# Performance work log

Hardware: AMD Instinct MI355X
Metric: run time of the kernel (lower is better)

Reference implementation:

```python
import jax, jax.numpy as jnp
import numpy as np

B, N, D, T = 32768, 20, 172, 100
E = D + T          # MHA embed dim = 272
H = 2              # num heads
HD = E // H        # head dim = 136
MEM = 172


def setup_inputs() -> dict:
    key = jax.random.key(0)
    ks = jax.random.split(key, 16)
    s = 0.02
    return {
        "message_batch": jax.random.normal(ks[0], (B, N, D), jnp.float32),
        "time_batch": jax.random.normal(ks[1], (B, N), jnp.float32),
        "memory": jax.random.normal(ks[2], (B, MEM), jnp.float32),
        # TimeEncode: Linear(1, T) -> weight [T], bias [T], output cos(w*t+b)
        "time_w": jax.random.normal(ks[3], (T,), jnp.float32),
        "time_b": jax.random.normal(ks[4], (T,), jnp.float32),
        # nn.MultiheadAttention(embed_dim=E, num_heads=2)
        "in_proj_w": jax.random.normal(ks[5], (3 * E, E), jnp.float32) * s,
        "in_proj_b": jnp.zeros((3 * E,), jnp.float32),
        "out_proj_w": jax.random.normal(ks[6], (E, E), jnp.float32) * s,
        "out_proj_b": jnp.zeros((E,), jnp.float32),
        # MergeLayer(E, D, D, D): fc1 Linear(E+D, D), fc2 Linear(D, D)
        "fc1_w": jax.random.normal(ks[7], (D, E + D), jnp.float32) * s,
        "fc1_b": jnp.zeros((D,), jnp.float32),
        "fc2_w": jax.random.normal(ks[8], (D, D), jnp.float32) * s,
        "fc2_b": jnp.zeros((D,), jnp.float32),
    }


def reference(message_batch, time_batch, memory, time_w, time_b,
              in_proj_w, in_proj_b, out_proj_w, out_proj_b,
              fc1_w, fc1_b, fc2_w, fc2_b):
    # --- aggregate() batched core (use_age=False) ---
    mask = time_batch < 0                              # [B,N] key_padding_mask (True = pad)
    source_time = time_batch[:, -1:]                   # [B,1]
    delta = time_batch - source_time                   # [B,N]
    # TimeEncode: cos(Linear(1->T))
    time_feat = jnp.cos(delta[..., None] * time_w + time_b)   # [B,N,T]

    # --- attention_node.forward ---
    msgs_un = jnp.concatenate([message_batch, time_feat], axis=-1)  # [B,N,E]
    source = message_batch[:, -1, :]                   # [B,D] (reassigned; memory unused for output)
    Q = jnp.concatenate([source, time_feat[:, -1, :]], axis=-1)    # [B,E]

    invalid = mask.all(axis=1)                         # [B] all-padded rows
    mask = mask.at[:, 0].set(jnp.where(invalid, False, mask[:, 0]))

    # nn.MultiheadAttention (self K=V)
    wq, wk, wv = in_proj_w[:E], in_proj_w[E:2 * E], in_proj_w[2 * E:]
    bq, bk, bv = in_proj_b[:E], in_proj_b[E:2 * E], in_proj_b[2 * E:]
    q = (Q @ wq.T + bq).reshape(B, H, HD)              # [B,H,hd]
    k = (msgs_un @ wk.T + bk).reshape(B, N, H, HD)     # [B,N,H,hd]
    v = (msgs_un @ wv.T + bv).reshape(B, N, H, HD)

    scale = 1.0 / jnp.sqrt(jnp.asarray(HD, q.dtype))
    scores = jnp.einsum("bhd,bnhd->bhn", q, k) * scale  # [B,H,N]
    neg = jnp.asarray(-1e9, scores.dtype)
    scores = jnp.where(mask[:, None, :], neg, scores)
    attn = jax.nn.softmax(scores, axis=-1)
    ctx = jnp.einsum("bhn,bnhd->bhd", attn, v).reshape(B, E)
    attn_out = ctx @ out_proj_w.T + out_proj_b          # [B,E]
    attn_out = jnp.where(invalid[:, None], 0.0, attn_out)

    # MergeLayer: fc2(relu(fc1(cat(attn_out, source))))
    h = jax.nn.relu(jnp.concatenate([attn_out, source], axis=-1) @ fc1_w.T + fc1_b)
    out = h @ fc2_w.T + fc2_b                           # [B,D] aggregated messages
    return out
```

## Files before the change

### kernel.cpp

```cpp
#include <hip/hip_runtime.h>
#include <math.h>

#define BB 32768
#define BN 20
#define DD 172
#define TT 100
#define EE 272
#define HD2 136
#define BT 16

#define XLD 448
#define QLD 548
#define NQK 546
#define GBM 128
#define GBN 128
#define GBK 64

#define GSWZ(k) ((((k) >> 3) & 7) << 2)

__global__ __launch_bounds__(256, 2)
void gemm_f32(const float* __restrict__ A, int lda,
              const float* __restrict__ W, int ldw,
              const float* __restrict__ bias,
              float* __restrict__ C, int ldc,
              int N, int K, int act, const int* __restrict__ inval)
{
  __shared__ float As[GBK][GBM + 4];
  __shared__ float Ws[GBK][GBN + 4];
  const int t  = threadIdx.x;
  const int bm = blockIdx.x * GBM;
  const int bn = blockIdx.y * GBN;
  const int tx = t & 15, ty = t >> 4;
  const int c4 = (t & 15) * 4;
  const int g4 = (t >> 4) * 4;

  float acc[8][8];
#pragma unroll
  for (int i = 0; i < 8; i++)
#pragma unroll
    for (int j = 0; j < 8; j++) acc[i][j] = 0.f;

  for (int kt = 0; kt < K; kt += GBK) {
    const int kg = kt + c4;
    const bool kv = (kg < K);
    const int sw = GSWZ(c4);

#pragma unroll
    for (int p = 0; p < 2; p++) {
      const int m0 = g4 + p * 64;
      float4 v0 = make_float4(0.f,0.f,0.f,0.f), v1 = v0, v2 = v0, v3 = v0;
      if (kv) {
        const float* ap = A + (size_t)(bm + m0) * lda + kg;
        v0 = *(const float4*)(ap);
        v1 = *(const float4*)(ap + lda);
        v2 = *(const float4*)(ap + 2 * (size_t)lda);
        v3 = *(const float4*)(ap + 3 * (size_t)lda);
      }
      const int ms = m0 ^ sw;
      *(float4*)&As[c4 + 0][ms] = make_float4(v0.x, v1.x, v2.x, v3.x);
      *(float4*)&As[c4 + 1][ms] = make_float4(v0.y, v1.y, v2.y, v3.y);
      *(float4*)&As[c4 + 2][ms] = make_float4(v0.z, v1.z, v2.z, v3.z);
      *(float4*)&As[c4 + 3][ms] = make_float4(v0.w, v1.w, v2.w, v3.w);
    }
#pragma unroll
    for (int p = 0; p < 2; p++) {
      const int n0 = g4 + p * 64;
      float4 v0 = make_float4(0.f,0.f,0.f,0.f), v1 = v0, v2 = v0, v3 = v0;
      if (kv) {
        const float* wp = W + (size_t)(bn + n0) * ldw + kg;
        if (bn + n0 + 0 < N) v0 = *(const float4*)(wp);
        if (bn + n0 + 1 < N) v1 = *(const float4*)(wp + ldw);
        if (bn + n0 + 2 < N) v2 = *(const float4*)(wp + 2 * (size_t)ldw);
        if (bn + n0 + 3 < N) v3 = *(const float4*)(wp + 3 * (size_t)ldw);
      }
      const int ns = n0 ^ sw;
      *(float4*)&Ws[c4 + 0][ns] = make_float4(v0.x, v1.x, v2.x, v3.x);
      *(float4*)&Ws[c4 + 1][ns] = make_float4(v0.y, v1.y, v2.y, v3.y);
      *(float4*)&Ws[c4 + 2][ns] = make_float4(v0.z, v1.z, v2.z, v3.z);
      *(float4*)&Ws[c4 + 3][ns] = make_float4(v0.w, v1.w, v2.w, v3.w);
    }
    __syncthreads();

#pragma unroll 4
    for (int k = 0; k < GBK; k++) {
      const int s = GSWZ(k);
      const float4 a0 = *(const float4*)&As[k][(ty * 4) ^ s];
      const float4 a1 = *(const float4*)&As[k][(64 + ty * 4) ^ s];
      const float4 b0 = *(const float4*)&Ws[k][(tx * 4) ^ s];
      const float4 b1 = *(const float4*)&Ws[k][(64 + tx * 4) ^ s];
      const float av[8] = {a0.x, a0.y, a0.z, a0.w, a1.x, a1.y, a1.z, a1.w};
      const float bv[8] = {b0.x, b0.y, b0.z, b0.w, b1.x, b1.y, b1.z, b1.w};
#pragma unroll
      for (int i = 0; i < 8; i++)
#pragma unroll
        for (int j = 0; j < 8; j++)
          acc[i][j] = fmaf(av[i], bv[j], acc[i][j]);
    }
    __syncthreads();
  }

#pragma unroll
  for (int i = 0; i < 8; i++) {
    const int row = bm + ((i < 4) ? (ty * 4 + i) : (64 + ty * 4 + i - 4));
    const int zr = (act == 2) ? inval[row] : 0;
#pragma unroll
    for (int jh = 0; jh < 2; jh++) {
      const int n0 = bn + jh * 64 + tx * 4;
      if (n0 < N) {
        const float4 bs = *(const float4*)(bias + n0);
        float4 v = make_float4(acc[i][jh * 4 + 0] + bs.x,
                               acc[i][jh * 4 + 1] + bs.y,
                               acc[i][jh * 4 + 2] + bs.z,
                               acc[i][jh * 4 + 3] + bs.w);
        if (act == 1) {
          v.x = fmaxf(v.x, 0.f); v.y = fmaxf(v.y, 0.f);
          v.z = fmaxf(v.z, 0.f); v.w = fmaxf(v.w, 0.f);
        }
        if (zr) { v.x = 0.f; v.y = 0.f; v.z = 0.f; v.w = 0.f; }
        *(float4*)(C + (size_t)row * ldc + n0) = v;
      }
    }
  }
}

__global__ __launch_bounds__(256)
void kprep0(const float* __restrict__ ipw, const float* __restrict__ ipb,
            const float* __restrict__ opw, const float* __restrict__ opb,
            const float* __restrict__ tbg,
            float* __restrict__ qconst, float* __restrict__ cvo)
{
  for (int e = threadIdx.x; e < EE; e += 256) {
    float s = ipb[e];
    for (int u = 0; u < TT; u++)
      s += cosf(tbg[u]) * ipw[(size_t)e * EE + DD + u];
    qconst[e] = s;
    float s2 = opb[e];
    for (int c = 0; c < EE; c++)
      s2 += ipb[2 * EE + c] * opw[(size_t)e * EE + c];
    cvo[e] = s2;
  }
}

#define NT1 (NQK * DD)
#define NT2 (NT1 + NQK)
#define NT3 (NT2 + EE * 2 * EE)

__global__ __launch_bounds__(256)
void kprep1(const float* __restrict__ ipw, const float* __restrict__ ipb,
            const float* __restrict__ opw, const float* __restrict__ qconst,
            float* __restrict__ wqk, float* __restrict__ cqk,
            float* __restrict__ wvo)
{
  for (int idx = blockIdx.x * 256 + threadIdx.x; idx < NT3;
       idx += gridDim.x * 256) {
    if (idx < NT1) {
      const int n = idx / DD, k = idx % DD;
      const int h = n / 273, j = n % 273;
      const float* wa = ipw + (size_t)(h * HD2) * EE + k;
      float s = 0.f;
      if (j < EE) {
        const float* wb = ipw + (size_t)(EE + h * HD2) * EE + j;
        for (int d = 0; d < HD2; d++) s += wa[(size_t)d * EE] * wb[(size_t)d * EE];
      } else {
        const float* bb = ipb + EE + h * HD2;
        for (int d = 0; d < HD2; d++) s += wa[(size_t)d * EE] * bb[d];
      }
      wqk[idx] = s;
    } else if (idx < NT2) {
      const int n = idx - NT1;
      const int h = n / 273, j = n % 273;
      const float* qc = qconst + h * HD2;
      float s = 0.f;
      if (j < EE) {
        const float* wb = ipw + (size_t)(EE + h * HD2) * EE + j;
        for (int d = 0; d < HD2; d++) s += qc[d] * wb[(size_t)d * EE];
      } else {
        const float* bb = ipb + EE + h * HD2;
        for (int d = 0; d < HD2; d++) s += qc[d] * bb[d];
      }
      cqk[n] = s;
    } else {
      const int r = idx - NT2;
      const int e = r / (2 * EE), kk = r % (2 * EE);
      const int h = kk / EE, j = kk % EE;
      const float* wv = ipw + (size_t)(2 * EE + h * HD2) * EE + j;
      const float* wo = opw + (size_t)e * EE + h * HD2;
      float s = 0.f;
      for (int d = 0; d < HD2; d++) s += wv[(size_t)d * EE] * wo[d];
      wvo[r] = s;
    }
  }
}

__global__ __launch_bounds__(256)
void ksrc(const float* __restrict__ msg, float* __restrict__ xbuf)
{
  const int total = BB * DD;
  for (int idx = blockIdx.x * 256 + threadIdx.x; idx < total;
       idx += gridDim.x * 256) {
    const int i = idx / DD, d = idx % DD;
    xbuf[(size_t)i * XLD + EE + d] =
        msg[((size_t)i * BN + (BN - 1)) * DD + d];
  }
}

__global__ __launch_bounds__(256, 2)
void attn_mid(const float* __restrict__ msg,
              const float* __restrict__ timeb,
              const float* __restrict__ twg,
              const float* __restrict__ tbg,
              float* __restrict__ qkbuf,
              int* __restrict__ inval)
{
  __shared__ float s_red[4][16][41];
  __shared__ float s_sc[4][40];
  const int t = threadIdx.x;
  const int w = t >> 6, l = t & 63;
  const size_t i = (size_t)blockIdx.x * 4 + w;

  const float* tbr = timeb + i * BN;
  float d[BN];
  unsigned msk = 0;
  const float st = tbr[BN - 1];
#pragma unroll
  for (int n = 0; n < BN; n++) {
    const float v = tbr[n];
    if (v < 0.f) msk |= (1u << n);
    d[n] = v - st;
  }
  const int inv = (msk == ((1u << BN) - 1u)) ? 1 : 0;
  if (inv) msk &= ~1u;

  const float w0 = twg[l], b0 = tbg[l];
  float w1 = 0.f, b1 = 0.f;
  if (l < TT - 64) { w1 = twg[64 + l]; b1 = tbg[64 + l]; }

  float* qkr = qkbuf + i * QLD;
  float qm0[2], qm1[2], qm2[2], qt0[2], qt1[2], sct[2];
#pragma unroll
  for (int h = 0; h < 2; h++) {
    const float* q = qkr + h * 273;
    qm0[h] = q[l];
    qm1[h] = q[64 + l];
    qm2[h] = (l < DD - 128) ? q[128 + l] : 0.f;
    qt0[h] = q[DD + l];
    qt1[h] = (l < TT - 64) ? q[DD + 64 + l] : 0.f;
    sct[h] = q[272];
  }

  const float* mrow = msg + i * (size_t)(BN * DD);
  float acc[2][BN];
#pragma unroll
  for (int n = 0; n < BN; n++) { acc[0][n] = 0.f; acc[1][n] = 0.f; }
#pragma unroll
  for (int n = 0; n < BN; n++) {
    const float m0 = mrow[n * DD + l];
    const float m1 = mrow[n * DD + 64 + l];
    const float m2 = (l < DD - 128) ? mrow[n * DD + 128 + l] : 0.f;
    const float c0 = __cosf(d[n] * w0 + b0);
    const float c1 = __cosf(d[n] * w1 + b1);
    acc[0][n] += m0 * qm0[0] + m1 * qm1[0] + m2 * qm2[0] + c0 * qt0[0] + c1 * qt1[0];
    acc[1][n] += m0 * qm0[1] + m1 * qm1[1] + m2 * qm2[1] + c0 * qt0[1] + c1 * qt1[1];
  }

  float* af = &acc[0][0];
#pragma unroll
  for (int x = 0; x < 40; x++) {
    float v = af[x];
    v += __shfl_xor(v, 32);
    v += __shfl_xor(v, 16);
    af[x] = v;
  }
  if (l < 16) {
#pragma unroll
    for (int x = 0; x < 40; x++) s_red[w][l][x] = af[x];
  }
  __syncthreads();
  if (l < 40) {
    float s = 0.f;
#pragma unroll
    for (int q = 0; q < 16; q++) s += s_red[w][q][l];
    const int h = (l >= BN) ? 1 : 0;
    const int n = l - h * BN;
    s += sct[h];
    s *= 0.08574929257125442f;
    if ((msk >> n) & 1u) s = -1e9f;
    s_sc[w][l] = s;
  }
  __syncthreads();

  float p[40];
#pragma unroll
  for (int x = 0; x < 40; x += 4) {
    const float4 v4 = *(const float4*)&s_sc[w][x];
    p[x] = v4.x; p[x + 1] = v4.y; p[x + 2] = v4.z; p[x + 3] = v4.w;
  }
#pragma unroll
  for (int h = 0; h < 2; h++) {
    float mx = p[h * BN];
#pragma unroll
    for (int n = 1; n < BN; n++) mx = fmaxf(mx, p[h * BN + n]);
    float sm = 0.f;
#pragma unroll
    for (int n = 0; n < BN; n++) {
      const float e = __expf(p[h * BN + n] - mx);
      p[h * BN + n] = e; sm += e;
    }
    const float is = 1.f / sm;
#pragma unroll
    for (int n = 0; n < BN; n++) p[h * BN + n] *= is;
  }

  float a0[2] = {0.f, 0.f}, a1[2] = {0.f, 0.f}, a2[2] = {0.f, 0.f};
  float t0[2] = {0.f, 0.f}, t1[2] = {0.f, 0.f};
#pragma unroll
  for (int n = 0; n < BN; n++) {
    const float m0 = mrow[n * DD + l];
    const float m1 = mrow[n * DD + 64 + l];
    const float m2 = (l < DD - 128) ? mrow[n * DD + 128 + l] : 0.f;
    const float c0 = __cosf(d[n] * w0 + b0);
    const float c1 = __cosf(d[n] * w1 + b1);
#pragma unroll
    for (int h = 0; h < 2; h++) {
      const float at = p[h * BN + n];
      a0[h] = fmaf(at, m0, a0[h]);
      a1[h] = fmaf(at, m1, a1[h]);
      a2[h] = fmaf(at, m2, a2[h]);
      t0[h] = fmaf(at, c0, t0[h]);
      t1[h] = fmaf(at, c1, t1[h]);
    }
  }
#pragma unroll
  for (int h = 0; h < 2; h++) {
    float* o = qkr + h * EE;
    o[l] = a0[h];
    o[64 + l] = a1[h];
    if (l < DD - 128) o[128 + l] = a2[h];
    o[DD + l] = t0[h];
    if (l < TT - 64) o[DD + 64 + l] = t1[h];
  }
  if (l == 0) inval[i] = inv;
}

__device__ __forceinline__ void gemm_rowW(
    const float* __restrict__ W, int ldw, int kcol0,
    const float* __restrict__ bias,
    const float* __restrict__ A, int lda,
    int K,
    float* OUT, int ldo, int NO,
    bool accum, int act,
    const int* __restrict__ inval,
    float* __restrict__ gout, int gld,
    int t)
{
  const int eo = t & 63;
  const int i0 = (t >> 6) * 4;
  for (int e = eo; e < NO; e += 128) {
    const int e2 = e + 64;
    const bool has2 = (e2 < NO);
    float acc[4][2];
    const float b1 = (!accum && bias) ? bias[e] : 0.f;
    const float b2 = (!accum && bias && has2) ? bias[e2] : 0.f;
#pragma unroll
    for (int ii = 0; ii < 4; ii++) {
      acc[ii][0] = accum ? OUT[(i0 + ii) * ldo + e] : b1;
      acc[ii][1] = has2 ? (accum ? OUT[(i0 + ii) * ldo + e2] : b2) : 0.f;
    }
    const float* w1 = W + (size_t)e * ldw + kcol0;
    const float* w2 = W + (size_t)e2 * ldw + kcol0;
    for (int k = 0; k < K; k += 4) {
      const float4 wq1 = *(const float4*)(w1 + k);
      float4 wq2 = make_float4(0.f, 0.f, 0.f, 0.f);
      if (has2) wq2 = *(const float4*)(w2 + k);
#pragma unroll
      for (int ii = 0; ii < 4; ii++) {
        const float4 a = *(const float4*)(A + (size_t)(i0 + ii) * lda + k);
        acc[ii][0] += a.x * wq1.x + a.y * wq1.y + a.z * wq1.z + a.w * wq1.w;
        acc[ii][1] += a.x * wq2.x + a.y * wq2.y + a.z * wq2.z + a.w * wq2.w;
      }
    }
#pragma unroll
    for (int ii = 0; ii < 4; ii++) {
      float v1 = acc[ii][0], v2 = acc[ii][1];
      if (act == 1) { v1 = fmaxf(v1, 0.f); v2 = fmaxf(v2, 0.f); }
      else if (act == 2) { if (inval[i0 + ii]) { v1 = 0.f; v2 = 0.f; } }
      if (gout) {
        gout[(i0 + ii) * gld + e] = v1;
        if (has2) gout[(i0 + ii) * gld + e2] = v2;
      } else {
        OUT[(i0 + ii) * ldo + e] = v1;
        if (has2) OUT[(i0 + ii) * ldo + e2] = v2;
      }
    }
  }
}

__device__ __forceinline__ void gemm_colW(
    const float* __restrict__ W, int ldw,
    const float* __restrict__ A, int lda,
    int K,
    float* OUT, int ldo, int NO,
    int t)
{
  const int eo = t & 63;
  const int i0 = (t >> 6) * 4;
  for (int j = eo; j < NO; j += 128) {
    const int j2 = j + 64;
    const bool has2 = (j2 < NO);
    float acc[4][2];
#pragma unroll
    for (int ii = 0; ii < 4; ii++) { acc[ii][0] = 0.f; acc[ii][1] = 0.f; }
    for (int dd = 0; dd < K; dd += 4) {
      const float* wr = W + (size_t)dd * ldw;
      const float w10 = wr[j];
      const float w11 = wr[ldw + j];
      const float w12 = wr[2 * ldw + j];
      const float w13 = wr[3 * ldw + j];
      float w20 = 0.f, w21 = 0.f, w22 = 0.f, w23 = 0.f;
      if (has2) { w20 = wr[j2]; w21 = wr[ldw + j2]; w22 = wr[2 * ldw + j2]; w23 = wr[3 * ldw + j2]; }
#pragma unroll
      for (int ii = 0; ii < 4; ii++) {
        const float4 a = *(const float4*)(A + (size_t)(i0 + ii) * lda + dd);
        acc[ii][0] += a.x * w10 + a.y * w11 + a.z * w12 + a.w * w13;
        acc[ii][1] += a.x * w20 + a.y * w21 + a.z * w22 + a.w * w23;
      }
    }
#pragma unroll
    for (int ii = 0; ii < 4; ii++) {
      OUT[(i0 + ii) * ldo + j] = acc[ii][0];
      if (has2) OUT[(i0 + ii) * ldo + j2] = acc[ii][1];
    }
  }
}

__global__ __launch_bounds__(256, 2)
void attn_msg_agg_fused(const float* __restrict__ msg,
                        const float* __restrict__ timeb,
                        const float* __restrict__ tw_g,
                        const float* __restrict__ tb_g,
                        const float* __restrict__ ipw,
                        const float* __restrict__ ipb,
                        const float* __restrict__ opw,
                        const float* __restrict__ opb,
                        const float* __restrict__ f1w,
                        const float* __restrict__ f1b,
                        const float* __restrict__ f2w,
                        const float* __restrict__ f2b,
                        float* __restrict__ outg)
{
  __shared__ __align__(16) float s_q[BT * EE];
  __shared__ __align__(16) float s_qk[BT * 2 * EE];
  __shared__ __align__(16) float s_attn[BT * 2 * BN];
  __shared__ __align__(16) float s_delta[BT * BN];
  __shared__ __align__(16) float s_tw[TT];
  __shared__ __align__(16) float s_tb[TT];
  __shared__ __align__(16) float s_tfl[TT];
  __shared__ float s_sconst[BT * 2];
  __shared__ unsigned s_mask[BT];
  __shared__ int s_inval[BT];

  const int t = threadIdx.x;
  const int base = blockIdx.x * BT;

  if (t < TT) {
    const float b = tb_g[t];
    s_tw[t] = tw_g[t];
    s_tb[t] = b;
    s_tfl[t] = __cosf(b);
  }
  for (int idx = t; idx < BT * BN; idx += 256)
    s_delta[idx] = timeb[(size_t)base * BN + idx];
  __syncthreads();
  if (t < BT) {
    const float st = s_delta[t * BN + BN - 1];
    unsigned m = 0;
#pragma unroll
    for (int n = 0; n < BN; n++) {
      const float v = s_delta[t * BN + n];
      if (v < 0.f) m |= (1u << n);
      s_delta[t * BN + n] = v - st;
    }
    const int inv = (m == ((1u << BN) - 1u)) ? 1 : 0;
    if (inv) m &= ~1u;
    s_mask[t] = m;
    s_inval[t] = inv;
  }
  __syncthreads();

  const float* srcA = msg + (size_t)base * BN * DD + (size_t)(BN - 1) * DD;
  gemm_rowW(ipw, EE, 0, ipb, srcA, BN * DD, DD, s_q, EE, EE, false, 0, nullptr, nullptr, 0, t);
  gemm_rowW(ipw, EE, DD, nullptr, s_tfl, 0, TT, s_q, EE, EE, true, 0, nullptr, nullptr, 0, t);
  __syncthreads();

  if (t < BT * 2) {
    const int i = t >> 1, h = t & 1;
    const float* qv = s_q + i * EE + h * HD2;
    const float* bk = ipb + EE + h * HD2;
    float s = 0.f;
    for (int dd = 0; dd < HD2; dd++) s += qv[dd] * bk[dd];
    s_sconst[t] = s;
  }
  gemm_colW(ipw + (size_t)EE * EE, EE, s_q, EE, HD2, s_qk, 2 * EE, EE, t);
  gemm_colW(ipw + (size_t)(EE + HD2) * EE, EE, s_q + HD2, EE, HD2, s_qk + EE, 2 * EE, EE, t);
  __syncthreads();

  const float scale = 0.08574929257125442f;
  for (int o = t; o < BT * 2 * BN; o += 256) {
    const int i = o / (2 * BN);
    const int r = o % (2 * BN);
    const int h = r / BN;
    const int n = r % BN;
    const float* mrow = msg + ((size_t)(base + i) * BN + n) * DD;
    const float* qkv = s_qk + i * 2 * EE + h * EE;
    float s = s_sconst[i * 2 + h];
    for (int dd = 0; dd < DD; dd += 4) {
      const float4 m4 = *(const float4*)(mrow + dd);
      const float4 q4 = *(const float4*)(qkv + dd);
      s += m4.x * q4.x + m4.y * q4.y + m4.z * q4.z + m4.w * q4.w;
    }
    const float del = s_delta[i * BN + n];
    const float* qkt = qkv + DD;
    for (int u = 0; u < TT; u++)
      s += __cosf(del * s_tw[u] + s_tb[u]) * qkt[u];
    const bool masked = (s_mask[i] >> n) & 1u;
    s_attn[o] = masked ? -1e9f : s * scale;
  }
  __syncthreads();

  if (t < BT * 2) {
    float* sc = s_attn + t * BN;
    float m = -3.4e38f;
#pragma unroll
    for (int n = 0; n < BN; n++) m = fmaxf(m, sc[n]);
    float sum = 0.f;
#pragma unroll
    for (int n = 0; n < BN; n++) { const float e = __expf(sc[n] - m); sc[n] = e; sum += e; }
    const float inv = 1.f / sum;
#pragma unroll
    for (int n = 0; n < BN; n++) sc[n] *= inv;
  }
  __syncthreads();

  for (int o = t; o < BT * 2 * EE; o += 256) {
    const int i = o / (2 * EE);
    const int r = o % (2 * EE);
    const int h = r / EE;
    const int j = r % EE;
    const float* at = s_attn + (i * 2 + h) * BN;
    float acc = 0.f;
    if (j < DD) {
      const float* mp = msg + (size_t)(base + i) * BN * DD + j;
#pragma unroll
      for (int n = 0; n < BN; n++) acc += at[n] * mp[n * DD];
    } else {
      const int u = j - DD;
      const float ww = s_tw[u], bb = s_tb[u];
#pragma unroll
      for (int n = 0; n < BN; n++) acc += at[n] * __cosf(s_delta[i * BN + n] * ww + bb);
    }
    s_qk[o] = acc;
  }
  __syncthreads();

  gemm_rowW(ipw + (size_t)(2 * EE) * EE, EE, 0, ipb + 2 * EE,
            s_qk, 2 * EE, EE, s_q, EE, HD2, false, 0, nullptr, nullptr, 0, t);
  gemm_rowW(ipw + (size_t)(2 * EE + HD2) * EE, EE, 0, ipb + 2 * EE + HD2,
            s_qk + EE, 2 * EE, EE, s_q + HD2, EE, HD2, false, 0, nullptr, nullptr, 0, t);
  __syncthreads();

  gemm_rowW(opw, EE, 0, opb, s_q, EE, EE, s_qk, 2 * EE, EE, false, 2, s_inval, nullptr, 0, t);
  __syncthreads();

  gemm_rowW(f1w, EE + DD, 0, f1b, s_qk, 2 * EE, EE, s_q, EE, DD, false, 0, nullptr, nullptr, 0, t);
  gemm_rowW(f1w, EE + DD, EE, nullptr, srcA, BN * DD, DD, s_q, EE, DD, true, 1, nullptr, nullptr, 0, t);
  __syncthreads();

  gemm_rowW(f2w, DD, 0, f2b, s_q, EE, DD, nullptr, 0, DD, false, 0, nullptr,
            outg + (size_t)base * DD, DD, t);
}

extern "C" void kernel_launch(void* const* d_in, const int* in_sizes, int n_in,
                              void* d_out, int out_size, void* d_ws, size_t ws_size,
                              hipStream_t stream) {
  const float* msg  = (const float*)d_in[0];
  const float* tb   = (const float*)d_in[1];
  const float* tw_g = (const float*)d_in[3];
  const float* tb_g = (const float*)d_in[4];
  const float* ipw  = (const float*)d_in[5];
  const float* ipb  = (const float*)d_in[6];
  const float* opw  = (const float*)d_in[7];
  const float* opb  = (const float*)d_in[8];
  const float* f1w  = (const float*)d_in[9];
  const float* f1b  = (const float*)d_in[10];
  const float* f2w  = (const float*)d_in[11];
  const float* f2b  = (const float*)d_in[12];
  float* outg = (float*)d_out;

  const size_t F_X   = 0;
  const size_t F_QK  = F_X   + (size_t)BB * XLD;
  const size_t F_WQK = F_QK  + (size_t)BB * QLD;
  const size_t F_CQK = F_WQK + (size_t)NQK * DD;
  const size_t F_WVO = F_CQK + 548;
  const size_t F_CVO = F_WVO + (size_t)EE * 2 * EE;
  const size_t F_QC  = F_CVO + EE;
  const size_t F_INV = F_QC  + EE;
  const size_t NEEDF = F_INV + BB;

  if (ws_size >= NEEDF * sizeof(float)) {
    float* ws    = (float*)d_ws;
    float* xbuf  = ws + F_X;
    float* qkb   = ws + F_QK;
    float* wqk   = ws + F_WQK;
    float* cqk   = ws + F_CQK;
    float* wvo   = ws + F_WVO;
    float* cvo   = ws + F_CVO;
    float* qc    = ws + F_QC;
    int*   inval = (int*)(ws + F_INV);

    hipLaunchKernelGGL(kprep0, dim3(1), dim3(256), 0, stream,
                       ipw, ipb, opw, opb, tb_g, qc, cvo);
    hipLaunchKernelGGL(kprep1, dim3(512), dim3(256), 0, stream,
                       ipw, ipb, opw, qc, wqk, cqk, wvo);
    hipLaunchKernelGGL(ksrc, dim3(2048), dim3(256), 0, stream, msg, xbuf);
    hipLaunchKernelGGL(gemm_f32, dim3(BB / GBM, 5), dim3(256), 0, stream,
                       xbuf + EE, XLD, wqk, DD, cqk, qkb, QLD,
                       NQK, DD, 0, (const int*)nullptr);
    hipLaunchKernelGGL(attn_mid, dim3(BB / 4), dim3(256), 0, stream,
                       msg, tb, tw_g, tb_g, qkb, inval);
    hipLaunchKernelGGL(gemm_f32, dim3(BB / GBM, 3), dim3(256), 0, stream,
                       qkb, QLD, wvo, 2 * EE, cvo, xbuf, XLD,
                       EE, 2 * EE, 2, inval);
    hipLaunchKernelGGL(gemm_f32, dim3(BB / GBM, 2), dim3(256), 0, stream,
                       xbuf, XLD, f1w, EE + DD, f1b, qkb, DD,
                       DD, EE + DD, 1, (const int*)nullptr);
    hipLaunchKernelGGL(gemm_f32, dim3(BB / GBM, 2), dim3(256), 0, stream,
                       qkb, DD, f2w, DD, f2b, outg, DD,
                       DD, DD, 0, (const int*)nullptr);
  } else {
    dim3 grid(BB / BT), block(256);
    hipLaunchKernelGGL(attn_msg_agg_fused, grid, block, 0, stream,
                       msg, tb, tw_g, tb_g, ipw, ipb, opw, opb,
                       f1w, f1b, f2w, f2b, outg);
  }
}
```

Measured before the change: 1.178 ms.

## Fold V/out-proj into fc1 weights and add register prefetch to GEMM

Precomputes a combined weight matrix that folds the value projection, output projection and the attention half of fc1 into one [D x 720] matrix. This replaces two batch-sized GEMMs (VO then fc1) with a single one over a unified buffer holding source, a validity column and the weighted context. Invalid rows are handled by scaling the context and bias column by a validity flag instead of masking in the epilogue. The GEMM gains templated N-width and register double-buffered global loads for the next K tile, at the cost of extra prep kernels and more register pressure.

```diff
diff --git a/kernel.cpp b/kernel.cpp
--- a/kernel.cpp
+++ b/kernel.cpp
@@ -9,91 +9,117 @@
 #define HD2 136
 #define BT 16
 
-#define XLD 448
-#define QLD 548
-#define NQK 546
+#define XLD2 728
+#define KMO  720
+#define QOFF 176
+#define NQK  546
+#define HLD  176
 #define GBM 128
-#define GBN 128
 #define GBK 64
 
 #define GSWZ(k) ((((k) >> 3) & 7) << 2)
 
+template<int PW>
+__device__ __forceinline__ void g_fetch(
+    const float* __restrict__ A, int lda,
+    const float* __restrict__ W, int ldw,
+    int N, int K, int bm, int bn, int kt, int c4, int g4,
+    float4 ra[2][4], float4 rw[PW][4])
+{
+  const int kg = kt + c4;
+  const bool kv = (kg < K);
+#pragma unroll
+  for (int p = 0; p < 2; p++) {
+    if (kv) {
+      const float* ap = A + (size_t)(bm + g4 + p * 64) * lda + kg;
+      ra[p][0] = *(const float4*)(ap);
+      ra[p][1] = *(const float4*)(ap + lda);
+      ra[p][2] = *(const float4*)(ap + 2 * (size_t)lda);
+      ra[p][3] = *(const float4*)(ap + 3 * (size_t)lda);
+    } else {
+      ra[p][0] = ra[p][1] = ra[p][2] = ra[p][3] = make_float4(0.f, 0.f, 0.f, 0.f);
+    }
+  }
+#pragma unroll
+  for (int p = 0; p < PW; p++) {
+    const int n0 = g4 + p * 64;
+    rw[p][0] = rw[p][1] = rw[p][2] = rw[p][3] = make_float4(0.f, 0.f, 0.f, 0.f);
+    if (kv) {
+      const float* wp = W + (size_t)(bn + n0) * ldw + kg;
+      if (bn + n0 + 0 < N) rw[p][0] = *(const float4*)(wp);
+      if (bn + n0 + 1 < N) rw[p][1] = *(const float4*)(wp + ldw);
+      if (bn + n0 + 2 < N) rw[p][2] = *(const float4*)(wp + 2 * (size_t)ldw);
+      if (bn + n0 + 3 < N) rw[p][3] = *(const float4*)(wp + 3 * (size_t)ldw);
+    }
+  }
+}
+
+template<int PW>
 __global__ __launch_bounds__(256, 2)
 void gemm_f32(const float* __restrict__ A, int lda,
               const float* __restrict__ W, int ldw,
               const float* __restrict__ bias,
               float* __restrict__ C, int ldc,
-              int N, int K, int act, const int* __restrict__ inval)
+              int N, int K, int act)
 {
   __shared__ float As[GBK][GBM + 4];
-  __shared__ float Ws[GBK][GBN + 4];
+  __shared__ float Ws[GBK][PW * 64 + 4];
   const int t  = threadIdx.x;
   const int bm = blockIdx.x * GBM;
-  const int bn = blockIdx.y * GBN;
+  const int bn = blockIdx.y * (PW * 64);
   const int tx = t & 15, ty = t >> 4;
   const int c4 = (t & 15) * 4;
   const int g4 = (t >> 4) * 4;
-
-  float acc[8][8];
+  const int sw0 = GSWZ(c4);
+
+  float acc[8][4 * PW];
 #pragma unroll
   for (int i = 0; i < 8; i++)
 #pragma unroll
-    for (int j = 0; j < 8; j++) acc[i][j] = 0.f;
+    for (int j = 0; j < 4 * PW; j++) acc[i][j] = 0.f;
+
+  float4 ra[2][4], rw[PW][4];
+  g_fetch<PW>(A, lda, W, ldw, N, K, bm, bn, 0, c4, g4, ra, rw);
 
   for (int kt = 0; kt < K; kt += GBK) {
-    const int kg = kt + c4;
-    const bool kv = (kg < K);
-    const int sw = GSWZ(c4);
-
 #pragma unroll
     for (int p = 0; p < 2; p++) {
-      const int m0 = g4 + p * 64;
-      float4 v0 = make_float4(0.f,0.f,0.f,0.f), v1 = v0, v2 = v0, v3 = v0;
-      if (kv) {
-        const float* ap = A + (size_t)(bm + m0) * lda + kg;
-        v0 = *(const float4*)(ap);
-        v1 = *(const float4*)(ap + lda);
-        v2 = *(const float4*)(ap + 2 * (size_t)lda);
-        v3 = *(const float4*)(ap + 3 * (size_t)lda);
-      }
-      const int ms = m0 ^ sw;
-      *(float4*)&As[c4 + 0][ms] = make_float4(v0.x, v1.x, v2.x, v3.x);
-      *(float4*)&As[c4 + 1][ms] = make_float4(v0.y, v1.y, v2.y, v3.y);
-      *(float4*)&As[c4 + 2][ms] = make_float4(v0.z, v1.z, v2.z, v3.z);
-      *(float4*)&As[c4 + 3][ms] = make_float4(v0.w, v1.w, v2.w, v3.w);
-    }
-#pragma unroll
-    for (int p = 0; p < 2; p++) {
-      const int n0 = g4 + p * 64;
-      float4 v0 = make_float4(0.f,0.f,0.f,0.f), v1 = v0, v2 = v0, v3 = v0;
-      if (kv) {
-        const float* wp = W + (size_t)(bn + n0) * ldw + kg;
-        if (bn + n0 + 0 < N) v0 = *(const float4*)(wp);
-        if (bn + n0 + 1 < N) v1 = *(const float4*)(wp + ldw);
-        if (bn + n0 + 2 < N) v2 = *(const float4*)(wp + 2 * (size_t)ldw);
-        if (bn + n0 + 3 < N) v3 = *(const float4*)(wp + 3 * (size_t)ldw);
-      }
-      const int ns = n0 ^ sw;
-      *(float4*)&Ws[c4 + 0][ns] = make_float4(v0.x, v1.x, v2.x, v3.x);
-      *(float4*)&Ws[c4 + 1][ns] = make_float4(v0.y, v1.y, v2.y, v3.y);
-      *(float4*)&Ws[c4 + 2][ns] = make_float4(v0.z, v1.z, v2.z, v3.z);
-      *(float4*)&Ws[c4 + 3][ns] = make_float4(v0.w, v1.w, v2.w, v3.w);
+      const int ms = (g4 + p * 64) ^ sw0;
+      *(float4*)&As[c4 + 0][ms] = make_float4(ra[p][0].x, ra[p][1].x, ra[p][2].x, ra[p][3].x);
+      *(float4*)&As[c4 + 1][ms] = make_float4(ra[p][0].y, ra[p][1].y, ra[p][2].y, ra[p][3].y);
+      *(float4*)&As[c4 + 2][ms] = make_float4(ra[p][0].z, ra[p][1].z, ra[p][2].z, ra[p][3].z);
+      *(float4*)&As[c4 + 3][ms] = make_float4(ra[p][0].w, ra[p][1].w, ra[p][2].w, ra[p][3].w);
+    }
+#pragma unroll
+    for (int p = 0; p < PW; p++) {
+      const int ns = (g4 + p * 64) ^ sw0;
+      *(float4*)&Ws[c4 + 0][ns] = make_float4(rw[p][0].x, rw[p][1].x, rw[p][2].x, rw[p][3].x);
+      *(float4*)&Ws[c4 + 1][ns] = make_float4(rw[p][0].y, rw[p][1].y, rw[p][2].y, rw[p][3].y);
+      *(float4*)&Ws[c4 + 2][ns] = make_float4(rw[p][0].z, rw[p][1].z, rw[p][2].z, rw[p][3].z);
+      *(float4*)&Ws[c4 + 3][ns] = make_float4(rw[p][0].w, rw[p][1].w, rw[p][2].w, rw[p][3].w);
     }
     __syncthreads();
+
+    if (kt + GBK < K)
+      g_fetch<PW>(A, lda, W, ldw, N, K, bm, bn, kt + GBK, c4, g4, ra, rw);
 
 #pragma unroll 4
     for (int k = 0; k < GBK; k++) {
       const int s = GSWZ(k);
       const float4 a0 = *(const float4*)&As[k][(ty * 4) ^ s];
       const float4 a1 = *(const float4*)&As[k][(64 + ty * 4) ^ s];
+      const float av[8] = {a0.x, a0.y, a0.z, a0.w, a1.x, a1.y, a1.z, a1.w};
+      float bv[4 * PW];
       const float4 b0 = *(const float4*)&Ws[k][(tx * 4) ^ s];
-      const float4 b1 = *(const float4*)&Ws[k][(64 + tx * 4) ^ s];
-      const float av[8] = {a0.x, a0.y, a0.z, a0.w, a1.x, a1.y, a1.z, a1.w};
-      const float bv[8] = {b0.x, b0.y, b0.z, b0.w, b1.x, b1.y, b1.z, b1.w};
+      bv[0] = b0.x; bv[1] = b0.y; bv[2] = b0.z; bv[3] = b0.w;
+      if constexpr (PW == 2) {
+        const float4 b1 = *(const float4*)&Ws[k][(64 + tx * 4) ^ s];
+        bv[4] = b1.x; bv[5] = b1.y; bv[6] = b1.z; bv[7] = b1.w;
+      }
 #pragma unroll
       for (int i = 0; i < 8; i++)
 #pragma unroll
-        for (int j = 0; j < 8; j++)
+        for (int j = 0; j < 4 * PW; j++)
           acc[i][j] = fmaf(av[i], bv[j], acc[i][j]);
     }
     __syncthreads();
@@ -102,9 +128,8 @@
 #pragma unroll
   for (int i = 0; i < 8; i++) {
     const int row = bm + ((i < 4) ? (ty * 4 + i) : (64 + ty * 4 + i - 4));
-    const int zr = (act == 2) ? inval[row] : 0;
-#pragma unroll
-    for (int jh = 0; jh < 2; jh++) {
+#pragma unroll
+    for (int jh = 0; jh < PW; jh++) {
       const int n0 = bn + jh * 64 + tx * 4;
       if (n0 < N) {
         const float4 bs = *(const float4*)(bias + n0);
@@ -116,7 +141,6 @@
           v.x = fmaxf(v.x, 0.f); v.y = fmaxf(v.y, 0.f);
           v.z = fmaxf(v.z, 0.f); v.w = fmaxf(v.w, 0.f);
         }
-        if (zr) { v.x = 0.f; v.y = 0.f; v.z = 0.f; v.w = 0.f; }
         *(float4*)(C + (size_t)row * ldc + n0) = v;
       }
     }
@@ -124,36 +148,32 @@
 }
 
 __global__ __launch_bounds__(256)
-void kprep0(const float* __restrict__ ipw, const float* __restrict__ ipb,
-            const float* __restrict__ opw, const float* __restrict__ opb,
-            const float* __restrict__ tbg,
-            float* __restrict__ qconst, float* __restrict__ cvo)
+void kprepA(const float* __restrict__ ipw, const float* __restrict__ ipb,
+            const float* __restrict__ tbg, float* __restrict__ qconst)
 {
   for (int e = threadIdx.x; e < EE; e += 256) {
     float s = ipb[e];
     for (int u = 0; u < TT; u++)
       s += cosf(tbg[u]) * ipw[(size_t)e * EE + DD + u];
     qconst[e] = s;
-    float s2 = opb[e];
-    for (int c = 0; c < EE; c++)
-      s2 += ipb[2 * EE + c] * opw[(size_t)e * EE + c];
-    cvo[e] = s2;
-  }
-}
-
-#define NT1 (NQK * DD)
-#define NT2 (NT1 + NQK)
-#define NT3 (NT2 + EE * 2 * EE)
+  }
+}
+
+#define PB0 (NQK * DD)
+#define PB1 (PB0 + NQK)
+#define PB2 (PB1 + DD * EE)
 
 __global__ __launch_bounds__(256)
-void kprep1(const float* __restrict__ ipw, const float* __restrict__ ipb,
-            const float* __restrict__ opw, const float* __restrict__ qconst,
+void kprepB(const float* __restrict__ ipw, const float* __restrict__ ipb,
+            const float* __restrict__ opw, const float* __restrict__ f1w,
+            const float* __restrict__ qconst,
             float* __restrict__ wqk, float* __restrict__ cqk,
-            float* __restrict__ wvo)
-{
-  for (int idx = blockIdx.x * 256 + threadIdx.x; idx < NT3;
+            float* __restrict__ Tm)
+{
+  if (blockIdx.x == 0 && threadIdx.x < 2) cqk[NQK + threadIdx.x] = 0.f;
+  for (int idx = blockIdx.x * 256 + threadIdx.x; idx < PB2;
        idx += gridDim.x * 256) {
-    if (idx < NT1) {
+    if (idx < PB0) {
       const int n = idx / DD, k = idx % DD;
       const int h = n / 273, j = n % 273;
       const float* wa = ipw + (size_t)(h * HD2) * EE + k;
@@ -166,8 +186,8 @@
         for (int d = 0; d < HD2; d++) s += wa[(size_t)d * EE] * bb[d];
       }
       wqk[idx] = s;
-    } else if (idx < NT2) {
-      const int n = idx - NT1;
+    } else if (idx < PB1) {
+      const int n = idx - PB0;
       const int h = n / 273, j = n % 273;
       const float* qc = qconst + h * HD2;
       float s = 0.f;
@@ -180,15 +200,47 @@
       }
       cqk[n] = s;
     } else {
-      const int r = idx - NT2;
-      const int e = r / (2 * EE), kk = r % (2 * EE);
-      const int h = kk / EE, j = kk % EE;
+      const int r = idx - PB1;
+      const int o = r / EE, c = r % EE;
+      const float* fa = f1w + (size_t)o * (EE + DD);
+      const float* wb = opw + c;
+      float s = 0.f;
+      for (int e = 0; e < EE; e++) s += fa[e] * wb[(size_t)e * EE];
+      Tm[r] = s;
+    }
+  }
+}
+
+#define PCN (DD * KMO)
+
+__global__ __launch_bounds__(256)
+void kprepC(const float* __restrict__ ipw, const float* __restrict__ ipb,
+            const float* __restrict__ opb, const float* __restrict__ f1w,
+            const float* __restrict__ Tm, float* __restrict__ wmof)
+{
+  for (int idx = blockIdx.x * 256 + threadIdx.x; idx < PCN;
+       idx += gridDim.x * 256) {
+    const int o = idx / KMO, kk = idx % KMO;
+    float s;
+    if (kk < DD) {
+      s = f1w[(size_t)o * (EE + DD) + EE + kk];
+    } else if (kk == DD) {
+      const float* fa = f1w + (size_t)o * (EE + DD);
+      const float* Tr = Tm + (size_t)o * EE;
+      s = 0.f;
+      for (int e = 0; e < EE; e++) s += fa[e] * opb[e];
+      for (int c = 0; c < EE; c++) s += Tr[c] * ipb[2 * EE + c];
+    } else if (kk < QOFF) {
+      s = 0.f;
+    } else {
+      const int j2 = kk - QOFF;
+      const int h = j2 / EE, j = j2 % EE;
+      const float* Tr = Tm + (size_t)o * EE + h * HD2;
       const float* wv = ipw + (size_t)(2 * EE + h * HD2) * EE + j;
-      const float* wo = opw + (size_t)e * EE + h * HD2;
-      float s = 0.f;
-      for (int d = 0; d < HD2; d++) s += wv[(size_t)d * EE] * wo[d];
-      wvo[r] = s;
-    }
+      s = 0.f;
+      for (int d = 0; d < HD2; d++) s += Tr[d] * wv[(size_t)d * EE];
+    }
+    wmof[idx] = s;
   }
 }
 
@@ -199,8 +251,7 @@
   for (int idx = blockIdx.x * 256 + threadIdx.x; idx < total;
        idx += gridDim.x * 256) {
     const int i = idx / DD, d = idx % DD;
-    xbuf[(size_t)i * XLD + EE + d] =
-        msg[((size_t)i * BN + (BN - 1)) * DD + d];
+    xbuf[(size_t)i * XLD2 + d] = msg[((size_t)i * BN + (BN - 1)) * DD + d];
   }
 }
 
@@ -209,8 +260,7 @@
               const float* __restrict__ timeb,
               const float* __restrict__ twg,
               const float* __restrict__ tbg,
-              float* __restrict__ qkbuf,
-              int* __restrict__ inval)
+              float* __restrict__ xbuf)
 {
   __shared__ float s_red[4][16][41];
   __shared__ float s_sc[4][40];
@@ -230,12 +280,14 @@
   }
   const int inv = (msk == ((1u << BN) - 1u)) ? 1 : 0;
   if (inv) msk &= ~1u;
+  const float vf = inv ? 0.f : 1.f;
 
   const float w0 = twg[l], b0 = tbg[l];
   float w1 = 0.f, b1 = 0.f;
   if (l < TT - 64) { w1 = twg[64 + l]; b1 = tbg[64 + l]; }
 
-  float* qkr = qkbuf + i * QLD;
+  float* xrow = xbuf + i * XLD2;
+  float* qkr = xrow + QOFF;
   float qm0[2], qm1[2], qm2[2], qt0[2], qt1[2], sct[2];
 #pragma unroll
   for (int h = 0; h < 2; h++) {
@@ -333,13 +385,18 @@
 #pragma unroll
   for (int h = 0; h < 2; h++) {
     float* o = qkr + h * EE;
-    o[l] = a0[h];
-    o[64 + l] = a1[h];
-    if (l < DD - 128) o[128 + l] = a2[h];
-    o[DD + l] = t0[h];
-    if (l < TT - 64) o[DD + 64 + l] = t1[h];
-  }
-  if (l == 0) inval[i] = inv;
+    o[l] = a0[h] * vf;
+    o[64 + l] = a1[h] * vf;
+    if (l < DD - 128) o[128 + l] = a2[h] * vf;
+    o[DD + l] = t0[h] * vf;
+    if (l < TT - 64) o[DD + 64 + l] = t1[h] * vf;
+  }
+  if (l == 0) {
+    xrow[DD] = vf;
+    xrow[DD + 1] = 0.f;
+    xrow[DD + 2] = 0.f;
+    xrow[DD + 3] = 0.f;
+  }
 }
 
 __device__ __forceinline__ void gemm_rowW(
@@ -596,46 +653,43 @@
   const float* f2b  = (const float*)d_in[12];
   float* outg = (float*)d_out;
 
-  const size_t F_X   = 0;
-  const size_t F_QK  = F_X   + (size_t)BB * XLD;
-  const size_t F_WQK = F_QK  + (size_t)BB * QLD;
-  const size_t F_CQK = F_WQK + (size_t)NQK * DD;
-  const size_t F_WVO = F_CQK + 548;
-  const size_t F_CVO = F_WVO + (size_t)EE * 2 * EE;
-  const size_t F_QC  = F_CVO + EE;
-  const size_t F_INV = F_QC  + EE;
-  const size_t NEEDF = F_INV + BB;
+  const size_t F_X    = 0;
+  const size_t F_H    = F_X    + (size_t)BB * XLD2;
+  const size_t F_WQK  = F_H    + (size_t)BB * HLD;
+  const size_t F_CQK  = F_WQK  + (size_t)NQK * DD;
+  const size_t F_T    = F_CQK  + 548;
+  const size_t F_WMOF = F_T    + (size_t)DD * EE;
+  const size_t F_QC   = F_WMOF + (size_t)DD * KMO;
+  const size_t NEEDF  = F_QC   + EE;
 
   if (ws_size >= NEEDF * sizeof(float)) {
-    float* ws    = (float*)d_ws;
-    float* xbuf  = ws + F_X;
-    float* qkb   = ws + F_QK;
-    float* wqk   = ws + F_WQK;
-    float* cqk   = ws + F_CQK;
-    float* wvo   = ws + F_WVO;
-    float* cvo   = ws + F_CVO;
-    float* qc    = ws + F_QC;
-    int*   inval = (int*)(ws + F_INV);
-
-    hipLaunchKernelGGL(kprep0, dim3(1), dim3(256), 0, stream,
-                       ipw, ipb, opw, opb, tb_g, qc, cvo);
-    hipLaunchKernelGGL(kprep1, dim3(512), dim3(256), 0, stream,
-                       ipw, ipb, opw, qc, wqk, cqk, wvo);
+    float* ws   = (float*)d_ws;
+    float* xbuf = ws + F_X;
+    float* hbuf = ws + F_H;
+    float* wqk  = ws + F_WQK;
+    float* cqk  = ws + F_CQK;
+    float* Tm   = ws + F_T;
+    float* wmof = ws + F_WMOF;
+    float* qc   = ws + F_QC;
+
+    hipLaunchKernelGGL(kprepA, dim3(1), dim3(256), 0, stream,
+                       ipw, ipb, tb_g, qc);
+    hipLaunchKernelGGL(kprepB, dim3(256), dim3(256), 0, stream,
+                       ipw, ipb, opw, f1w, qc, wqk, cqk, Tm);
+    hipLaunchKernelGGL(kprepC, dim3(256), dim3(256), 0, stream,
+                       ipw, ipb, opb, f1w, Tm, wmof);
     hipLaunchKernelGGL(ksrc, dim3(2048), dim3(256), 0, stream, msg, xbuf);
-    hipLaunchKernelGGL(gemm_f32, dim3(BB / GBM, 5), dim3(256), 0, stream,
-                       xbuf + EE, XLD, wqk, DD, cqk, qkb, QLD,
-                       NQK, DD, 0, (const int*)nullptr);
+    hipLaunchKernelGGL(gemm_f32<2>, dim3(BB / GBM, 5), dim3(256), 0, stream,
+                       xbuf, XLD2, wqk, DD, cqk, xbuf + QOFF, XLD2,
+                       NQK, DD, 0);
     hipLaunchKernelGGL(attn_mid, dim3(BB / 4), dim3(256), 0, stream,
-                       msg, tb, tw_g, tb_g, qkb, inval);
-    hipLaunchKernelGGL(gemm_f32, dim3(BB / GBM, 3), dim3(256), 0, stream,
-                       qkb, QLD, wvo, 2 * EE, cvo, xbuf, XLD,
-                       EE, 2 * EE, 2, inval);
-    hipLaunchKernelGGL(gemm_f32, dim3(BB / GBM, 2), dim3(256), 0, stream,
-                       xbuf, XLD, f1w, EE + DD, f1b, qkb, DD,
-                       DD, EE + DD, 1, (const int*)nullptr);
-    hipLaunchKernelGGL(gemm_f32, dim3(BB / GBM, 2), dim3(256), 0, stream,
-                       qkb, DD, f2w, DD, f2b, outg, DD,
-                       DD, DD, 0, (const int*)nullptr);
+                       msg, tb, tw_g, tb_g, xbuf);
+    hipLaunchKernelGGL(gemm_f32<1>, dim3(BB / GBM, 3), dim3(256), 0, stream,
+                       xbuf, XLD2, wmof, KMO, f1b, hbuf, HLD,
+                       DD, KMO, 1);
+    hipLaunchKernelGGL(gemm_f32<1>, dim3(BB / GBM, 3), dim3(256), 0, stream,
+                       hbuf, HLD, f2w, DD, f2b, outg, DD,
+                       DD, DD, 0);
   } else {
     dim3 grid(BB / BT), block(256);
     hipLaunchKernelGGL(attn_msg_agg_fused, grid, block, 0, stream,
```

Result: faster. 1.075 ms (-8.7%).
